# Optimization experiments

Measured on AMD Instinct MI355X. Metric: run time of the kernel, lower is better.

## Reference

```python
import jax, jax.numpy as jnp
import numpy as np
from jax import lax

B, N, C_IN, C_OUT = 4, 8192, 64, 128
STRIDE, RADIUS, K, L = 4, 0.1, 32, 2
EPS = 1e-5
M = N // STRIDE


def _bn(x, g, b):
    # training-mode batch norm, channel-first layout (B, C, ...)
    axes = (0,) + tuple(range(2, x.ndim))
    mean = jnp.mean(x, axis=axes, keepdims=True)
    var = jnp.mean((x - mean) ** 2, axis=axes, keepdims=True)
    sh = (1, -1) + (1,) * (x.ndim - 2)
    return (x - mean) * lax.rsqrt(var + EPS) * g.reshape(sh) + b.reshape(sh)


def _fps(points, m):
    # farthest point sampling starting at index 0 (matches fps_cuda semantics)
    b, n, _ = points.shape
    bi = jnp.arange(b)

    def body(carry, _):
        dis, last = carry
        lp = points[bi, last]  # (b,3)
        d = jnp.sum((points - lp[:, None, :]) ** 2, -1)
        dis = jnp.minimum(dis, d)
        return (dis, jnp.argmax(dis, -1).astype(jnp.int32)), last

    init = (jnp.full((b, n), 1e10, points.dtype), jnp.zeros((b,), jnp.int32))
    _, idx = lax.scan(body, init, None, length=m)
    return idx.T  # (b, m)


def _ball_query(radius, k, centroids, points, features):
    # first k points within radius of each centroid; pad with first hit
    b, n, _ = points.shape
    d2 = jnp.sum((centroids[:, :, None, :] - points[:, None, :, :]) ** 2, -1)  # (b,m,n)
    key = jnp.where(d2 < radius * radius, jnp.arange(n, dtype=jnp.int32), n)
    neg, _ = lax.top_k(-key, k)  # k smallest keys = first k in-ball indices
    sel = -neg  # (b,m,k)
    sel = jnp.where(sel == n, sel[..., :1], sel)
    sel = jnp.clip(sel, 0, n - 1)
    bi = jnp.arange(b)[:, None, None]
    gp = jnp.transpose(points[bi, sel], (0, 3, 2, 1))  # (b,3,k,m)
    gf = None
    if features is not None:
        gf = jnp.transpose(features[bi, sel], (0, 3, 2, 1))  # (b,c,k,m)
    return gp, gf


def _forward(pos, x, p):
    b, n, _ = pos.shape
    m = n // STRIDE
    bi = jnp.arange(b)[:, None]
    fps_idx = _fps(pos, m)
    centroids = pos[bi, fps_idx]  # (b,m,3)
    # x_mlp: 1x1 conv + BN + ReLU
    f = jax.nn.relu(_bn(jnp.einsum('bnc,oc->bon', x, p['W_x']), p['g_x'], p['b_x']))
    feats = jnp.transpose(f, (0, 2, 1))  # (b,n,C_OUT)
    gp, gf = _ball_query(RADIUS, K, centroids, pos, feats)
    cT = jnp.transpose(centroids, (0, 2, 1))[:, :, None, :]  # (b,3,1,m)
    gp = (gp - cT) / RADIUS
    gp = jax.nn.relu(_bn(jnp.einsum('bckm,oc->bokm', gp, p['W_ps']), p['g_ps'], p['b_ps']))
    xf = jnp.transpose(jnp.max(gf + gp, axis=2), (0, 2, 1))  # (b,m,C_OUT)
    # gen_pe on downsampled points
    R2 = RADIUS * 2
    gpe, _ = _ball_query(R2, K, centroids, centroids, None)
    gpe = (gpe - cT) / R2
    pe = jax.nn.relu(_bn(jnp.einsum('bckm,oc->bokm', gpe, p['W_pe']), p['g_pe'], p['b_pe']))
    # InvResMLP blocks
    for i in range(L):
        xc = jnp.transpose(xf, (0, 2, 1))  # (b,C,m)
        xc = jax.nn.relu(_bn(jnp.einsum('bcm,oc->bom', xc, p['W1'][i]), p['g1'][i], p['b1'][i]))
        feats_i = jnp.transpose(xc, (0, 2, 1))  # (b,m,C)
        _, gfi = _ball_query(R2, K, centroids, centroids, feats_i)
        g = jnp.max(gfi + pe, axis=2)  # (b,C,m)
        g = jax.nn.relu(_bn(jnp.einsum('bcm,oc->bom', g, p['W2a'][i]), p['g2a'][i], p['b2a'][i]))
        g = _bn(jnp.einsum('bcm,oc->bom', g, p['W2b'][i]), p['g2b'][i], p['b2b'][i])
        xf = jax.nn.relu(feats_i + jnp.transpose(g, (0, 2, 1)))
    return centroids, xf


def setup_inputs() -> dict:
    key = jax.random.key(0)
    ks = jax.random.split(key, 12)
    d = {
        'pos': jax.random.uniform(ks[0], (B, N, 3), jnp.float32),
        'x': jax.random.normal(ks[1], (B, N, C_IN), jnp.float32),
        'W_x': jax.random.normal(ks[2], (C_OUT, C_IN), jnp.float32) * 0.05,
        'g_x': jnp.ones((C_OUT,), jnp.float32), 'b_x': jnp.zeros((C_OUT,), jnp.float32),
        'W_ps': jax.random.normal(ks[3], (C_OUT, 3), jnp.float32) * 0.1,
        'g_ps': jnp.ones((C_OUT,), jnp.float32), 'b_ps': jnp.zeros((C_OUT,), jnp.float32),
        'W_pe': jax.random.normal(ks[4], (C_OUT, 3), jnp.float32) * 0.1,
        'g_pe': jnp.ones((C_OUT,), jnp.float32), 'b_pe': jnp.zeros((C_OUT,), jnp.float32),
        'W1': jax.random.normal(ks[5], (L, C_OUT, C_OUT), jnp.float32) * 0.05,
        'g1': jnp.ones((L, C_OUT), jnp.float32), 'b1': jnp.zeros((L, C_OUT), jnp.float32),
        'W2a': jax.random.normal(ks[6], (L, C_OUT, C_OUT), jnp.float32) * 0.05,
        'g2a': jnp.ones((L, C_OUT), jnp.float32), 'b2a': jnp.zeros((L, C_OUT), jnp.float32),
        'W2b': jax.random.normal(ks[7], (L, C_OUT, C_OUT), jnp.float32) * 0.05,
        'g2b': jnp.ones((L, C_OUT), jnp.float32), 'b2b': jnp.zeros((L, C_OUT), jnp.float32),
    }
    return d


def reference(pos, x, W_x, g_x, b_x, W_ps, g_ps, b_ps, W_pe, g_pe, b_pe,
              W1, g1, b1, W2a, g2a, b2a, W2b, g2b, b2b):
    p = dict(W_x=W_x, g_x=g_x, b_x=b_x, W_ps=W_ps, g_ps=g_ps, b_ps=b_ps,
             W_pe=W_pe, g_pe=g_pe, b_pe=b_pe, W1=W1, g1=g1, b1=b1,
             W2a=W2a, g2a=g2a, b2a=b2a, W2b=W2b, g2b=g2b, b2b=b2b)
    return _forward(pos, x, p)
```

## Files before the change

### kernel.cpp

```cpp
#include <hip/hip_runtime.h>


#define BB 4
#define NN 8192
#define MM 2048
#define HM 1024
#define KK 32
#define CI 64
#define CO 128
#define SG 16

typedef float vf2 __attribute__((ext_vector_type(2)));

#define ST_X 0
#define MO_PS 256
#define MO_PE 272
#define ST1 288
#define ST2A (288 + 2 * SG * 256)
#define ST2B (ST2A + 2 * SG * 256)
#define ST_TOTAL (ST2B + 512)

__device__ __forceinline__ float sq3(float dx, float dy, float dz) {
#pragma clang fp contract(off)
  return dx * dx + dy * dy + dz * dz;
}

__device__ __forceinline__ void fin_stats_d(const double* st, float gam,
                                            float bet, double cnt, int ch,
                                            float* sc, float* sh) {
  double mean = st[ch] / cnt;
  double var = st[128 + ch] / cnt - mean * mean;
  if (var < 0) var = 0;
  double s = (double)gam / sqrt(var + 1e-5);
  *sc = (float)s;
  *sh = (float)((double)bet - mean * s);
}

__device__ __forceinline__ void fin_grp_d(const double* st, float gam,
                                          float bet, double cnt, int ch,
                                          float* sc, float* sh) {
  double sum = 0, ssq = 0;
#pragma unroll
  for (int g = 0; g < SG; g++) {
    sum += st[g * 256 + ch];
    ssq += st[g * 256 + 128 + ch];
  }
  double mean = sum / cnt;
  double var = ssq / cnt - mean * mean;
  if (var < 0) var = 0;
  double s = (double)gam / sqrt(var + 1e-5);
  *sc = (float)s;
  *sh = (float)((double)bet - mean * s);
}

__device__ __forceinline__ void fin_mom_d(const double* mo, const float* Wrow,
                                          float gam, float bet, double cnt,
                                          float* sc, float* sh) {
  double w0 = Wrow[0], w1 = Wrow[1], w2 = Wrow[2];
  double mx = mo[0] / cnt, my = mo[1] / cnt, mz = mo[2] / cnt;
  double sxx = mo[3] / cnt, sxy = mo[4] / cnt, sxz = mo[5] / cnt;
  double syy = mo[6] / cnt, syz = mo[7] / cnt, szz = mo[8] / cnt;
  double mean = w0 * mx + w1 * my + w2 * mz;
  double ey2 = w0 * w0 * sxx + w1 * w1 * syy + w2 * w2 * szz +
               2.0 * (w0 * w1 * sxy + w0 * w2 * sxz + w1 * w2 * syz);
  double var = ey2 - mean * mean;
  if (var < 0) var = 0;
  double s = (double)gam / sqrt(var + 1e-5);
  *sc = (float)s;
  *sh = (float)((double)bet - mean * s);
}

template <int CTRL>
__device__ __forceinline__ int dpp_i(int v) {
  return __builtin_amdgcn_update_dpp(v, v, CTRL, 0xF, 0xF, false);
}
template <int CTRL>
__device__ __forceinline__ float dpp_f(float v) {
  return __int_as_float(dpp_i<CTRL>(__float_as_int(v)));
}

#define FT 512
#define NP 8
#define NW 8

__device__ __forceinline__ void bq_wave(int pair, const float* __restrict__ pts,
                                        int npts, float rsq, float inv_r,
                                        int* __restrict__ sel,
                                        const float* __restrict__ cent,
                                        int lane, int* __restrict__ s_selw,
                                        float* __restrict__ s_momw) {
  int b = pair >> 11;
  const float* P = pts + (size_t)b * npts * 3;
  const float* C = cent + (size_t)pair * 3;
  float cx = C[0], cy = C[1], cz = C[2];
  int cnt = 0;
  unsigned long long ltm = (1ull << lane) - 1ull;
  int nit = npts >> 8;
  for (int ch = 0; ch < nit; ch++) {
    int i0 = (ch << 8) + lane;
    bool h0, h1, h2, h3;
    {
      float a0 = P[i0 * 3 + 0], a1 = P[i0 * 3 + 1], a2 = P[i0 * 3 + 2];
      float b0 = P[(i0 + 64) * 3 + 0], b1 = P[(i0 + 64) * 3 + 1],
            b2 = P[(i0 + 64) * 3 + 2];
      float c0 = P[(i0 + 128) * 3 + 0], c1 = P[(i0 + 128) * 3 + 1],
            c2 = P[(i0 + 128) * 3 + 2];
      float e0 = P[(i0 + 192) * 3 + 0], e1 = P[(i0 + 192) * 3 + 1],
            e2 = P[(i0 + 192) * 3 + 2];
      h0 = sq3(a0 - cx, a1 - cy, a2 - cz) < rsq;
      h1 = sq3(b0 - cx, b1 - cy, b2 - cz) < rsq;
      h2 = sq3(c0 - cx, c1 - cy, c2 - cz) < rsq;
      h3 = sq3(e0 - cx, e1 - cy, e2 - cz) < rsq;
    }
    unsigned long long m0 = __ballot(h0);
    unsigned long long m1 = __ballot(h1);
    unsigned long long m2 = __ballot(h2);
    unsigned long long m3 = __ballot(h3);
    if (m0) {
      int k = cnt + __popcll(m0 & ltm);
      if (h0 && k < KK) s_selw[k] = i0;
      cnt += __popcll(m0);
    }
    if (m1) {
      int k = cnt + __popcll(m1 & ltm);
      if (h1 && k < KK) s_selw[k] = i0 + 64;
      cnt += __popcll(m1);
    }
    if (m2) {
      int k = cnt + __popcll(m2 & ltm);
      if (h2 && k < KK) s_selw[k] = i0 + 128;
      cnt += __popcll(m2);
    }
    if (m3) {
      int k = cnt + __popcll(m3 & ltm);
      if (h3 && k < KK) s_selw[k] = i0 + 192;
      cnt += __popcll(m3);
    }
    if (cnt >= KK) break;
  }
  int total = cnt < KK ? cnt : KK;
  int myidx = 0;
  if (lane < KK) {
    int v = (lane < total) ? s_selw[lane] : s_selw[0];
    sel[(size_t)pair * KK + lane] = v;
    myidx = v;
  }
  float gx = 0.f, gy = 0.f, gz = 0.f;
  if (lane < KK) {
    gx = (P[myidx * 3 + 0] - cx) * inv_r;
    gy = (P[myidx * 3 + 1] - cy) * inv_r;
    gz = (P[myidx * 3 + 2] - cz) * inv_r;
  }
  float v9[9] = {gx, gy, gz, gx * gx, gx * gy, gx * gz, gy * gy, gy * gz,
                 gz * gz};
#pragma unroll
  for (int j = 0; j < 9; j++) {
#pragma unroll
    for (int off = 32; off > 0; off >>= 1) v9[j] += __shfl_xor(v9[j], off);
  }
  if (lane == 0) {
#pragma unroll
    for (int j = 0; j < 9; j++) s_momw[j] = v9[j];
  }
}

__global__ __launch_bounds__(FT) void k_fps_conv(
    const float* __restrict__ pos, const float* __restrict__ x,
    const float* __restrict__ W_x, float* __restrict__ cent,
    float* __restrict__ fpre, double* __restrict__ stats,
    float* __restrict__ gds) {
  __shared__ alignas(16) unsigned long long s_key[2][NW];
  __shared__ alignas(16) float s_pts[NN * 3];
  __shared__ alignas(16) float s_cent[MM * 3];
  int t = threadIdx.x;
  if (blockIdx.x >= BB) {
    int cb = blockIdx.x - BB;
    int o = t & 127, q = t >> 7;
    float4 w[CI / 4];
    const float4* Wv = (const float4*)(W_x + (size_t)o * CI);
#pragma unroll
    for (int i = 0; i < CI / 4; i++) w[i] = Wv[i];
    int row0 = cb * 128;
    float ssum = 0.f, ssq = 0.f;
    for (int r = 0; r < 128; r += 4) {
      int row = __builtin_amdgcn_readfirstlane(row0 + r + q);
      const float* xr = x + (size_t)row * CI;
      float acc = 0.f;
#pragma unroll
      for (int i = 0; i < CI / 4; i++) {
        float4 a = *(const float4*)(xr + 4 * i);
        acc += a.x * w[i].x + a.y * w[i].y + a.z * w[i].z + a.w * w[i].w;
      }
      fpre[(size_t)row * CO + o] = acc;
      ssum += acc;
      ssq += acc * acc;
    }
    atomicAdd(&stats[ST_X + o], (double)ssum);
    atomicAdd(&stats[ST_X + 128 + o], (double)ssq);
    return;
  }
  int b = blockIdx.x;
  const float* P = pos + (size_t)b * NN * 3;
  float* C = cent + (size_t)b * MM * 3;
  int lane = t & 63, w = t >> 6;
  int ws = __builtin_amdgcn_readfirstlane(w);
  for (int i = t; i < (NN * 3) / 4; i += FT) {
    ((float4*)s_pts)[i] = ((const float4*)P)[i];
  }
  vf2 px[NP], py[NP], pz[NP], ds[NP];
#pragma unroll
  for (int s = 0; s < NP; s++) {
    int ia = (2 * s) * FT + t;
    int ib = ia + FT;
    px[s] = (vf2){P[ia * 3 + 0], P[ib * 3 + 0]};
    py[s] = (vf2){P[ia * 3 + 1], P[ib * 3 + 1]};
    pz[s] = (vf2){P[ia * 3 + 2], P[ib * 3 + 2]};
    ds[s] = (vf2){1e10f, 1e10f};
  }
  float lx = P[0], ly = P[1], lz = P[2];
  if (t == 0) {
    s_cent[0] = lx;
    s_cent[1] = ly;
    s_cent[2] = lz;
  }
  __syncthreads();
  for (int m = 1; m < HM; m++) {
    vf2 l2x = (vf2){lx, lx}, l2y = (vf2){ly, ly}, l2z = (vf2){lz, lz};
    vf2 bmax = (vf2){-1.0f, -1.0f};
    {
#pragma clang fp contract(off)
#pragma unroll
      for (int s = 0; s < NP; s++) {
        vf2 dx = px[s] - l2x;
        vf2 dy = py[s] - l2y;
        vf2 dz = pz[s] - l2z;
        vf2 d2 = dx * dx + dy * dy + dz * dz;
        vf2 nd = __builtin_elementwise_min(ds[s], d2);
        ds[s] = nd;
        bmax = __builtin_elementwise_max(bmax, nd);
      }
    }
    float bv = fmaxf(bmax.x, bmax.y);
    bv = fmaxf(bv, dpp_f<0x111>(bv));
    bv = fmaxf(bv, dpp_f<0x112>(bv));
    bv = fmaxf(bv, dpp_f<0x114>(bv));
    bv = fmaxf(bv, dpp_f<0x118>(bv));
    bv = fmaxf(bv, dpp_f<0x142>(bv));
    bv = fmaxf(bv, dpp_f<0x143>(bv));
    float wmax =
        __int_as_float(__builtin_amdgcn_readlane(__float_as_int(bv), 63));
    unsigned idxw = 0xffffffffu;
#pragma unroll
    for (int s = NP - 1; s >= 0; s--) {
      unsigned long long mby = __ballot(ds[s].y == wmax);
      unsigned basey = (unsigned)((2 * s) * FT + FT + (ws << 6));
      if (mby) idxw = basey + (unsigned)(__ffsll((long long)mby) - 1);
      unsigned long long mbx = __ballot(ds[s].x == wmax);
      unsigned basex = (unsigned)((2 * s) * FT + (ws << 6));
      if (mbx) idxw = basex + (unsigned)(__ffsll((long long)mbx) - 1);
    }
    int pb = m & 1;
    if (lane == 0) {
      s_key[pb][ws] = ((unsigned long long)__float_as_uint(wmax) << 32) |
                      (unsigned long long)(~idxw);
    }
    __syncthreads();
    const ulonglong2* kp = (const ulonglong2*)(&s_key[pb][0]);
    ulonglong2 q0 = kp[0];
    ulonglong2 q1 = kp[1];
    ulonglong2 q2 = kp[2];
    ulonglong2 q3 = kp[3];
    unsigned long long a0 = q0.x > q0.y ? q0.x : q0.y;
    unsigned long long a1 = q1.x > q1.y ? q1.x : q1.y;
    unsigned long long a2 = q2.x > q2.y ? q2.x : q2.y;
    unsigned long long a3 = q3.x > q3.y ? q3.x : q3.y;
    a0 = a0 > a1 ? a0 : a1;
    a2 = a2 > a3 ? a2 : a3;
    unsigned long long kw = a0 > a2 ? a0 : a2;
    unsigned gidx = ~(unsigned)(kw & 0xffffffffull);
    lx = s_pts[gidx * 3 + 0];
    ly = s_pts[gidx * 3 + 1];
    lz = s_pts[gidx * 3 + 2];
    if (t == 0) {
      s_cent[m * 3 + 0] = lx;
      s_cent[m * 3 + 1] = ly;
      s_cent[m * 3 + 2] = lz;
    }
  }
  __syncthreads();
  for (int i = t; i < (HM * 3) / 4; i += FT) {
    ((float4*)C)[i] = ((const float4*)s_cent)[i];
  }
  float2* gd = (float2*)gds + (size_t)b * NP * FT;
#pragma unroll
  for (int s = 0; s < NP; s++) {
    float2 v;
    v.x = ds[s].x;
    v.y = ds[s].y;
    gd[s * FT + t] = v;
  }
}

__global__ __launch_bounds__(FT) void k_fps_bq(const float* __restrict__ pos,
                                               float* __restrict__ cent,
                                               const float* __restrict__ gds,
                                               int* __restrict__ sel1,
                                               double* __restrict__ stats) {
  __shared__ alignas(16) unsigned long long s_key[2][NW];
  __shared__ alignas(16) float s_pts[NN * 3];
  __shared__ alignas(16) float s_cent[MM * 3];
  __shared__ int s_sel[NW][KK];
  __shared__ float s_mom[NW][9];
  int t = threadIdx.x;
  int lane = t & 63, w = t >> 6;
  if (blockIdx.x >= BB) {
    int pi = (blockIdx.x - BB) * 8 + w;
    int bb = pi >> 10, mi = pi & (HM - 1);
    int pair = bb * MM + mi;
    bq_wave(pair, pos, NN, 0.01f, 10.0f, sel1, cent, lane, s_sel[w],
            s_mom[w]);
    __syncthreads();
    if (t < 9) {
      double a = (double)s_mom[0][t];
#pragma unroll
      for (int j = 1; j < NW; j++) a += s_mom[j][t];
      atomicAdd(&stats[MO_PS + t], a);
    }
    return;
  }
  int b = blockIdx.x;
  const float* P = pos + (size_t)b * NN * 3;
  float* C = cent + (size_t)b * MM * 3;
  int ws = __builtin_amdgcn_readfirstlane(w);
  for (int i = t; i < (NN * 3) / 4; i += FT) {
    ((float4*)s_pts)[i] = ((const float4*)P)[i];
  }
  vf2 px[NP], py[NP], pz[NP], ds[NP];
  const float2* gd = (const float2*)gds + (size_t)b * NP * FT;
#pragma unroll
  for (int s = 0; s < NP; s++) {
    int ia = (2 * s) * FT + t;
    int ib = ia + FT;
    px[s] = (vf2){P[ia * 3 + 0], P[ib * 3 + 0]};
    py[s] = (vf2){P[ia * 3 + 1], P[ib * 3 + 1]};
    pz[s] = (vf2){P[ia * 3 + 2], P[ib * 3 + 2]};
    float2 v = gd[s * FT + t];
    ds[s] = (vf2){v.x, v.y};
  }
  float lx = C[(HM - 1) * 3 + 0];
  float ly = C[(HM - 1) * 3 + 1];
  float lz = C[(HM - 1) * 3 + 2];
  __syncthreads();
  for (int m = HM; m < MM; m++) {
    vf2 l2x = (vf2){lx, lx}, l2y = (vf2){ly, ly}, l2z = (vf2){lz, lz};
    vf2 bmax = (vf2){-1.0f, -1.0f};
    {
#pragma clang fp contract(off)
#pragma unroll
      for (int s = 0; s < NP; s++) {
        vf2 dx = px[s] - l2x;
        vf2 dy = py[s] - l2y;
        vf2 dz = pz[s] - l2z;
        vf2 d2 = dx * dx + dy * dy + dz * dz;
        vf2 nd = __builtin_elementwise_min(ds[s], d2);
        ds[s] = nd;
        bmax = __builtin_elementwise_max(bmax, nd);
      }
    }
    float bv = fmaxf(bmax.x, bmax.y);
    bv = fmaxf(bv, dpp_f<0x111>(bv));
    bv = fmaxf(bv, dpp_f<0x112>(bv));
    bv = fmaxf(bv, dpp_f<0x114>(bv));
    bv = fmaxf(bv, dpp_f<0x118>(bv));
    bv = fmaxf(bv, dpp_f<0x142>(bv));
    bv = fmaxf(bv, dpp_f<0x143>(bv));
    float wmax =
        __int_as_float(__builtin_amdgcn_readlane(__float_as_int(bv), 63));
    unsigned idxw = 0xffffffffu;
#pragma unroll
    for (int s = NP - 1; s >= 0; s--) {
      unsigned long long mby = __ballot(ds[s].y == wmax);
      unsigned basey = (unsigned)((2 * s) * FT + FT + (ws << 6));
      if (mby) idxw = basey + (unsigned)(__ffsll((long long)mby) - 1);
      unsigned long long mbx = __ballot(ds[s].x == wmax);
      unsigned basex = (unsigned)((2 * s) * FT + (ws << 6));
      if (mbx) idxw = basex + (unsigned)(__ffsll((long long)mbx) - 1);
    }
    int pb = m & 1;
    if (lane == 0) {
      s_key[pb][ws] = ((unsigned long long)__float_as_uint(wmax) << 32) |
                      (unsigned long long)(~idxw);
    }
    __syncthreads();
    const ulonglong2* kp = (const ulonglong2*)(&s_key[pb][0]);
    ulonglong2 q0 = kp[0];
    ulonglong2 q1 = kp[1];
    ulonglong2 q2 = kp[2];
    ulonglong2 q3 = kp[3];
    unsigned long long a0 = q0.x > q0.y ? q0.x : q0.y;
    unsigned long long a1 = q1.x > q1.y ? q1.x : q1.y;
    unsigned long long a2 = q2.x > q2.y ? q2.x : q2.y;
    unsigned long long a3 = q3.x > q3.y ? q3.x : q3.y;
    a0 = a0 > a1 ? a0 : a1;
    a2 = a2 > a3 ? a2 : a3;
    unsigned long long kw = a0 > a2 ? a0 : a2;
    unsigned gidx = ~(unsigned)(kw & 0xffffffffull);
    lx = s_pts[gidx * 3 + 0];
    ly = s_pts[gidx * 3 + 1];
    lz = s_pts[gidx * 3 + 2];
    if (t == 0) {
      s_cent[m * 3 + 0] = lx;
      s_cent[m * 3 + 1] = ly;
      s_cent[m * 3 + 2] = lz;
    }
  }
  __syncthreads();
  for (int i = t + (HM * 3) / 4; i < (MM * 3) / 4; i += FT) {
    ((float4*)C)[i] = ((const float4*)s_cent)[i];
  }
}

__global__ __launch_bounds__(256) void k_bq_rest(const float* __restrict__ pos,
                                                 const float* __restrict__ cent,
                                                 int* __restrict__ sel1,
                                                 int* __restrict__ sel2,
                                                 double* __restrict__ stats) {
  __shared__ int s_sel[4][KK];
  __shared__ float s_mom[4][9];
  int t = threadIdx.x, lane = t & 63, w = t >> 6;
  const float* pts;
  int npts, pair, mo;
  float rsq, inv_r;
  int* sel;
  if (blockIdx.x < (BB * HM) / 4) {
    int pi = blockIdx.x * 4 + w;
    int bb = pi >> 10, mi = pi & (HM - 1);
    pair = bb * MM + HM + mi;
    pts = pos;
    npts = NN;
    rsq = 0.01f;
    inv_r = 10.0f;
    sel = sel1;
    mo = MO_PS;
  } else {
    pair = (blockIdx.x - (BB * HM) / 4) * 4 + w;
    pts = cent;
    npts = MM;
    rsq = 0.04f;
    inv_r = 5.0f;
    sel = sel2;
    mo = MO_PE;
  }
  bq_wave(pair, pts, npts, rsq, inv_r, sel, cent, lane, s_sel[w], s_mom[w]);
  __syncthreads();
  if (t < 9) {
    double a = (double)s_mom[0][t] + s_mom[1][t] + s_mom[2][t] + s_mom[3][t];
    atomicAdd(&stats[mo + t], a);
  }
}

__global__ __launch_bounds__(128) void k_xf_conv1(
    const float* __restrict__ pos, const float* __restrict__ cent,
    const int* __restrict__ sel1, const float* __restrict__ fpre,
    const float* __restrict__ Wps, const float* __restrict__ g_ps,
    const float* __restrict__ b_ps, const float* __restrict__ g_x,
    const float* __restrict__ b_x, const double* __restrict__ stats,
    const float* __restrict__ W1, float* __restrict__ y1a,
    double* __restrict__ st1out) {
  int pair = blockIdx.x;
  int b = pair >> 11;
  int o = threadIdx.x;
  float sx, hx, sp, hp;
  fin_stats_d(stats + ST_X, g_x[o], b_x[o], (double)(BB * NN), o, &sx, &hx);
  fin_mom_d(stats + MO_PS, Wps + o * 3, g_ps[o], b_ps[o],
            (double)(BB * MM * KK), &sp, &hp);
  float w0 = Wps[o * 3 + 0], w1 = Wps[o * 3 + 1], w2 = Wps[o * 3 + 2];
  const float* C = cent + (size_t)pair * 3;
  float cx = C[0], cy = C[1], cz = C[2];
  const float* P = pos + (size_t)b * NN * 3;
  const float* F = fpre + (size_t)b * NN * CO;
  __shared__ int s_idx[KK];
  __shared__ float s_xf[128];
  if (o < KK) s_idx[o] = sel1[(size_t)pair * KK + o];
  __syncthreads();
  float acc = -1e30f;
#pragma unroll 4
  for (int k = 0; k < KK; k++) {
    int idx = __builtin_amdgcn_readfirstlane(s_idx[k]);
    float gx = (P[idx * 3 + 0] - cx) * 10.0f;
    float gy = (P[idx * 3 + 1] - cy) * 10.0f;
    float gz = (P[idx * 3 + 2] - cz) * 10.0f;
    float y = fmaxf((w0 * gx + w1 * gy + w2 * gz) * sp + hp, 0.f);
    float f = fmaxf(F[(size_t)idx * CO + o] * sx + hx, 0.f);
    float v = y + f;
    acc = v > acc ? v : acc;
  }
  s_xf[o] = acc;
  __syncthreads();
  const float4* Wv = (const float4*)(W1 + (size_t)o * CO);
  const float4* gv = (const float4*)s_xf;
  float dot = 0.f;
#pragma unroll
  for (int i = 0; i < CO / 4; i++) {
    float4 a = gv[i];
    float4 ww = Wv[i];
    dot += a.x * ww.x + a.y * ww.y + a.z * ww.z + a.w * ww.w;
  }
  y1a[(size_t)pair * CO + o] = dot;
  int grp = pair & (SG - 1);
  atomicAdd(&st1out[grp * 256 + o], (double)dot);
  atomicAdd(&st1out[grp * 256 + 128 + o], (double)(dot * dot));
}

__global__ __launch_bounds__(256) void k_conv_bnin(
    const float* __restrict__ in, const float* __restrict__ W,
    const double* __restrict__ st_grp, const float* __restrict__ gam,
    const float* __restrict__ bet, float* __restrict__ out,
    double* __restrict__ stats, int rows_per_block) {
  __shared__ float s_sc[128], s_sh[128];
  int t = threadIdx.x;
  if (t < 128) {
    fin_grp_d(st_grp, gam[t], bet[t], (double)(BB * MM), t, &s_sc[t],
              &s_sh[t]);
  }
  __syncthreads();
  int o = t & 127, half = t >> 7;
  float4 w[CO / 4];
  const float4* Wv = (const float4*)(W + (size_t)o * CO);
#pragma unroll
  for (int i = 0; i < CO / 4; i++) w[i] = Wv[i];
  int row0 = blockIdx.x * rows_per_block;
  float ssum = 0.f, ssq = 0.f;
  for (int r = 0; r < rows_per_block; r += 2) {
    int row = __builtin_amdgcn_readfirstlane(row0 + r + half);
    const float* xr = in + (size_t)row * CO;
    float acc = 0.f;
#pragma unroll
    for (int i = 0; i < CO / 4; i++) {
      float4 a = *(const float4*)(xr + 4 * i);
      a.x = fmaxf(a.x * s_sc[4 * i + 0] + s_sh[4 * i + 0], 0.f);
      a.y = fmaxf(a.y * s_sc[4 * i + 1] + s_sh[4 * i + 1], 0.f);
      a.z = fmaxf(a.z * s_sc[4 * i + 2] + s_sh[4 * i + 2], 0.f);
      a.w = fmaxf(a.w * s_sc[4 * i + 3] + s_sh[4 * i + 3], 0.f);
      acc += a.x * w[i].x + a.y * w[i].y + a.z * w[i].z + a.w * w[i].w;
    }
    out[(size_t)row * CO + o] = acc;
    ssum += acc;
    ssq += acc * acc;
  }
  atomicAdd(&stats[o], (double)ssum);
  atomicAdd(&stats[128 + o], (double)ssq);
}

__global__ __launch_bounds__(256) void k_conv_resid(
    const float* __restrict__ y1prev, const float* __restrict__ y2bprev,
    const double* __restrict__ st1p, const float* __restrict__ g1p,
    const float* __restrict__ b1p, const double* __restrict__ st2bp,
    const float* __restrict__ g2bp, const float* __restrict__ b2bp,
    const float* __restrict__ W, float* __restrict__ y1out,
    double* __restrict__ stats, int rows_per_block) {
  __shared__ float s_s1[128], s_h1[128], s_s2[128], s_h2[128];
  int t = threadIdx.x;
  if (t < 128) {
    fin_grp_d(st1p, g1p[t], b1p[t], (double)(BB * MM), t, &s_s1[t], &s_h1[t]);
    fin_stats_d(st2bp, g2bp[t], b2bp[t], (double)(BB * MM), t, &s_s2[t],
                &s_h2[t]);
  }
  __syncthreads();
  int o = t & 127, half = t >> 7;
  float4 w[CO / 4];
  const float4* Wv = (const float4*)(W + (size_t)o * CO);
#pragma unroll
  for (int i = 0; i < CO / 4; i++) w[i] = Wv[i];
  int row0 = blockIdx.x * rows_per_block;
  float ssum = 0.f, ssq = 0.f;
  for (int r = 0; r < rows_per_block; r += 2) {
    int row = __builtin_amdgcn_readfirstlane(row0 + r + half);
    const float* ar = y1prev + (size_t)row * CO;
    const float* br = y2bprev + (size_t)row * CO;
    float acc = 0.f;
#pragma unroll
    for (int i = 0; i < CO / 4; i++) {
      float4 a = *(const float4*)(ar + 4 * i);
      float4 bb = *(const float4*)(br + 4 * i);
      float x0 = fmaxf(fmaxf(a.x * s_s1[4 * i + 0] + s_h1[4 * i + 0], 0.f) +
                           (bb.x * s_s2[4 * i + 0] + s_h2[4 * i + 0]), 0.f);
      float x1 = fmaxf(fmaxf(a.y * s_s1[4 * i + 1] + s_h1[4 * i + 1], 0.f) +
                           (bb.y * s_s2[4 * i + 1] + s_h2[4 * i + 1]), 0.f);
      float x2 = fmaxf(fmaxf(a.z * s_s1[4 * i + 2] + s_h1[4 * i + 2], 0.f) +
                           (bb.z * s_s2[4 * i + 2] + s_h2[4 * i + 2]), 0.f);
      float x3 = fmaxf(fmaxf(a.w * s_s1[4 * i + 3] + s_h1[4 * i + 3], 0.f) +
                           (bb.w * s_s2[4 * i + 3] + s_h2[4 * i + 3]), 0.f);
      acc += x0 * w[i].x + x1 * w[i].y + x2 * w[i].z + x3 * w[i].w;
    }
    y1out[(size_t)row * CO + o] = acc;
    ssum += acc;
    ssq += acc * acc;
  }
  int grp = blockIdx.x & (SG - 1);
  atomicAdd(&stats[grp * 256 + o], (double)ssum);
  atomicAdd(&stats[grp * 256 + 128 + o], (double)ssq);
}

__global__ __launch_bounds__(128) void k_gconv(
    const float* __restrict__ cent, const int* __restrict__ sel2,
    const float* __restrict__ y1in, const double* __restrict__ st1,
    const float* __restrict__ g1v, const float* __restrict__ b1v,
    const double* __restrict__ mo_pe, const float* __restrict__ Wpe,
    const float* __restrict__ gpe, const float* __restrict__ bpe,
    const float* __restrict__ W2a, float* __restrict__ y2a,
    double* __restrict__ st2a) {
  int pair = blockIdx.x;
  int b = pair >> 11;
  int o = threadIdx.x;
  float s1, h1, se, he;
  fin_grp_d(st1, g1v[o], b1v[o], (double)(BB * MM), o, &s1, &h1);
  fin_mom_d(mo_pe, Wpe + o * 3, gpe[o], bpe[o], (double)(BB * MM * KK), &se,
            &he);
  float w0 = Wpe[o * 3 + 0], w1 = Wpe[o * 3 + 1], w2 = Wpe[o * 3 + 2];
  const float* C = cent + (size_t)pair * 3;
  float cx = C[0], cy = C[1], cz = C[2];
  const float* CB = cent + (size_t)b * MM * 3;
  const float* Y = y1in + (size_t)b * MM * CO;
  __shared__ int s_idx[KK];
  __shared__ float s_g[128];
  if (o < KK) s_idx[o] = sel2[(size_t)pair * KK + o];
  __syncthreads();
  float acc = -1e30f;
#pragma unroll 4
  for (int k = 0; k < KK; k++) {
    int idx = __builtin_amdgcn_readfirstlane(s_idx[k]);
    float gx = (CB[idx * 3 + 0] - cx) * 5.0f;
    float gy = (CB[idx * 3 + 1] - cy) * 5.0f;
    float gz = (CB[idx * 3 + 2] - cz) * 5.0f;
    float pe = fmaxf((w0 * gx + w1 * gy + w2 * gz) * se + he, 0.f);
    float f = fmaxf(Y[(size_t)idx * CO + o] * s1 + h1, 0.f);
    float v = pe + f;
    acc = v > acc ? v : acc;
  }
  s_g[o] = acc;
  __syncthreads();
  const float4* Wv = (const float4*)(W2a + (size_t)o * CO);
  const float4* gv = (const float4*)s_g;
  float dot = 0.f;
#pragma unroll
  for (int i = 0; i < CO / 4; i++) {
    float4 a = gv[i];
    float4 ww = Wv[i];
    dot += a.x * ww.x + a.y * ww.y + a.z * ww.z + a.w * ww.w;
  }
  y2a[(size_t)pair * CO + o] = dot;
  int grp = pair & (SG - 1);
  atomicAdd(&st2a[grp * 256 + o], (double)dot);
  atomicAdd(&st2a[grp * 256 + 128 + o], (double)(dot * dot));
}

__global__ __launch_bounds__(256) void k_resid_fin(
    const float* __restrict__ y1b, const double* __restrict__ st1,
    const float* __restrict__ g1v, const float* __restrict__ b1v,
    const float* __restrict__ y2b, const double* __restrict__ st2b,
    const float* __restrict__ g2bv, const float* __restrict__ b2bv,
    float* __restrict__ xf) {
  int i = blockIdx.x * 256 + threadIdx.x;
  int o = i & 127;
  float s1, h1, s2, h2;
  fin_grp_d(st1, g1v[o], b1v[o], (double)(BB * MM), o, &s1, &h1);
  fin_stats_d(st2b, g2bv[o], b2bv[o], (double)(BB * MM), o, &s2, &h2);
  float f = fmaxf(y1b[i] * s1 + h1, 0.f);
  float v = y2b[i] * s2 + h2;
  xf[i] = fmaxf(f + v, 0.f);
}

extern "C" void kernel_launch(void* const* d_in, const int* in_sizes, int n_in,
                              void* d_out, int out_size, void* d_ws,
                              size_t ws_size, hipStream_t stream) {
  const float* pos = (const float*)d_in[0];
  const float* x = (const float*)d_in[1];
  const float* W_x = (const float*)d_in[2];
  const float* g_x = (const float*)d_in[3];
  const float* b_x = (const float*)d_in[4];
  const float* W_ps = (const float*)d_in[5];
  const float* g_ps = (const float*)d_in[6];
  const float* b_ps = (const float*)d_in[7];
  const float* W_pe = (const float*)d_in[8];
  const float* g_pe = (const float*)d_in[9];
  const float* b_pe = (const float*)d_in[10];
  const float* W1 = (const float*)d_in[11];
  const float* g1 = (const float*)d_in[12];
  const float* b1 = (const float*)d_in[13];
  const float* W2a = (const float*)d_in[14];
  const float* g2a = (const float*)d_in[15];
  const float* b2a = (const float*)d_in[16];
  const float* W2b = (const float*)d_in[17];
  const float* g2b = (const float*)d_in[18];
  const float* b2b = (const float*)d_in[19];

  float* cent = (float*)d_out;
  float* xf = cent + (size_t)BB * MM * 3;

  char* p = (char*)d_ws;
  double* stats = (double*)p; p += (size_t)ST_TOTAL * sizeof(double);
  int* sel1 = (int*)p;        p += (size_t)BB * MM * KK * sizeof(int);
  int* sel2 = (int*)p;        p += (size_t)BB * MM * KK * sizeof(int);
  float* fpre = (float*)p;    p += (size_t)BB * NN * CO * sizeof(float);
  float* y1a = (float*)p;     p += (size_t)BB * MM * CO * sizeof(float);
  float* y1b = (float*)p;     p += (size_t)BB * MM * CO * sizeof(float);
  float* y2a = (float*)p;     p += (size_t)BB * MM * CO * sizeof(float);
  float* y2b = (float*)p;     p += (size_t)BB * MM * CO * sizeof(float);
  float* gds = (float*)p;     p += (size_t)BB * NP * FT * 2 * sizeof(float);

  hipMemsetAsync(stats, 0, (size_t)ST_TOTAL * sizeof(double), stream);
  k_fps_conv<<<BB + 256, FT, 0, stream>>>(pos, x, W_x, cent, fpre, stats, gds);
  k_fps_bq<<<BB + (BB * HM) / 8, FT, 0, stream>>>(pos, cent, gds, sel1, stats);
  k_bq_rest<<<(BB * HM) / 4 + (BB * MM) / 4, 256, 0, stream>>>(pos, cent, sel1,
                                                               sel2, stats);
  k_xf_conv1<<<BB * MM, 128, 0, stream>>>(pos, cent, sel1, fpre, W_ps, g_ps,
                                          b_ps, g_x, b_x, stats, W1, y1a,
                                          stats + ST1);
  k_gconv<<<BB * MM, 128, 0, stream>>>(cent, sel2, y1a, stats + ST1, g1, b1,
                                       stats + MO_PE, W_pe, g_pe, b_pe, W2a,
                                       y2a, stats + ST2A);
  k_conv_bnin<<<128, 256, 0, stream>>>(y2a, W2b, stats + ST2A, g2a, b2a, y2b,
                                       stats + ST2B, 64);
  k_conv_resid<<<128, 256, 0, stream>>>(
      y1a, y2b, stats + ST1, g1, b1, stats + ST2B, g2b, b2b, W1 + CO * CO, y1b,
      stats + ST1 + SG * 256, 64);
  k_gconv<<<BB * MM, 128, 0, stream>>>(cent, sel2, y1b, stats + ST1 + SG * 256,
                                       g1 + 128, b1 + 128, stats + MO_PE, W_pe,
                                       g_pe, b_pe, W2a + CO * CO, y2a,
                                       stats + ST2A + SG * 256);
  k_conv_bnin<<<128, 256, 0, stream>>>(y2a, W2b + CO * CO,
                                       stats + ST2A + SG * 256, g2a + 128,
                                       b2a + 128, y2b, stats + ST2B + 256, 64);
  k_resid_fin<<<(BB * MM * CO) / 256, 256, 0, stream>>>(
      y1b, stats + ST1 + SG * 256, g1 + 128, b1 + 128, y2b,
      stats + ST2B + 256, g2b + 128, b2b + 128, xf);
}
```

Before: 2.544 ms.

## Fuse tail stages into one cooperative persistent kernel with grid syncs

Replaces the eight tail kernels (remaining ball query, grouped convs, conv+BN layers, residual finalize) with one cooperative kernel of 256 blocks × 512 threads that steps through the stages separated by grid.sync. Each block now handles 32 pairs or rows, and per-block shared-memory reductions cut the number of double atomics on the stats buffers. The aim is to remove launch gaps and tail effects between many small kernels. In exchange, the grid is limited to 256 blocks, which lowers parallelism in the gather-heavy stages, and each stage boundary now costs a grid barrier.

```diff
diff --git a/kernel.cpp b/kernel.cpp
--- a/kernel.cpp
+++ b/kernel.cpp
@@ -1,4 +1,7 @@
 #include <hip/hip_runtime.h>
+#include <hip/hip_cooperative_groups.h>
+
+namespace cg = cooperative_groups;
 
 
 #define BB 4
@@ -9,6 +12,9 @@
 #define CI 64
 #define CO 128
 #define SG 16
+
+#define TB 256
+#define TT 512
 
 typedef float vf2 __attribute__((ext_vector_type(2)));
 
@@ -420,119 +426,102 @@
   }
 }
 
-__global__ __launch_bounds__(256) void k_bq_rest(const float* __restrict__ pos,
-                                                 const float* __restrict__ cent,
-                                                 int* __restrict__ sel1,
-                                                 int* __restrict__ sel2,
-                                                 double* __restrict__ stats) {
-  __shared__ int s_sel[4][KK];
-  __shared__ float s_mom[4][9];
-  int t = threadIdx.x, lane = t & 63, w = t >> 6;
-  const float* pts;
-  int npts, pair, mo;
-  float rsq, inv_r;
-  int* sel;
-  if (blockIdx.x < (BB * HM) / 4) {
-    int pi = blockIdx.x * 4 + w;
-    int bb = pi >> 10, mi = pi & (HM - 1);
-    pair = bb * MM + HM + mi;
-    pts = pos;
-    npts = NN;
-    rsq = 0.01f;
-    inv_r = 10.0f;
-    sel = sel1;
-    mo = MO_PS;
-  } else {
-    pair = (blockIdx.x - (BB * HM) / 4) * 4 + w;
-    pts = cent;
-    npts = MM;
-    rsq = 0.04f;
-    inv_r = 5.0f;
-    sel = sel2;
-    mo = MO_PE;
-  }
-  bq_wave(pair, pts, npts, rsq, inv_r, sel, cent, lane, s_sel[w], s_mom[w]);
+
+__device__ __forceinline__ void tail_gconv(
+    unsigned char* smem, int bid, int t, const float* __restrict__ cent,
+    const int* __restrict__ sel2, const float* __restrict__ yin,
+    const double* __restrict__ st1p, const float* __restrict__ g1v,
+    const float* __restrict__ b1v, const double* __restrict__ stats,
+    const float* __restrict__ Wpe, const float* __restrict__ gpe,
+    const float* __restrict__ bpe, const float* __restrict__ W2a_,
+    float* __restrict__ y2a_, double* __restrict__ st2a_) {
+  float* s_s1 = (float*)smem;
+  float* s_h1 = s_s1 + 128;
+  float* s_se = s_h1 + 128;
+  float* s_he = s_se + 128;
+  float* s_w0 = s_he + 128;
+  float* s_w1 = s_w0 + 128;
+  float* s_w2 = s_w1 + 128;
+  int* s_idx = (int*)(s_w2 + 128);
+  float* s_g = (float*)(s_idx + 4 * KK);
+  if (t < 128) {
+    float s1, h1, se, he;
+    fin_grp_d(st1p, g1v[t], b1v[t], (double)(BB * MM), t, &s1, &h1);
+    fin_mom_d(stats + MO_PE, Wpe + t * 3, gpe[t], bpe[t],
+              (double)(BB * MM * KK), &se, &he);
+    s_s1[t] = s1;
+    s_h1[t] = h1;
+    s_se[t] = se;
+    s_he[t] = he;
+    s_w0[t] = Wpe[t * 3 + 0];
+    s_w1[t] = Wpe[t * 3 + 1];
+    s_w2[t] = Wpe[t * 3 + 2];
+  }
   __syncthreads();
-  if (t < 9) {
-    double a = (double)s_mom[0][t] + s_mom[1][t] + s_mom[2][t] + s_mom[3][t];
-    atomicAdd(&stats[mo + t], a);
-  }
-}
-
-__global__ __launch_bounds__(128) void k_xf_conv1(
-    const float* __restrict__ pos, const float* __restrict__ cent,
-    const int* __restrict__ sel1, const float* __restrict__ fpre,
-    const float* __restrict__ Wps, const float* __restrict__ g_ps,
-    const float* __restrict__ b_ps, const float* __restrict__ g_x,
-    const float* __restrict__ b_x, const double* __restrict__ stats,
-    const float* __restrict__ W1, float* __restrict__ y1a,
-    double* __restrict__ st1out) {
-  int pair = blockIdx.x;
-  int b = pair >> 11;
-  int o = threadIdx.x;
-  float sx, hx, sp, hp;
-  fin_stats_d(stats + ST_X, g_x[o], b_x[o], (double)(BB * NN), o, &sx, &hx);
-  fin_mom_d(stats + MO_PS, Wps + o * 3, g_ps[o], b_ps[o],
-            (double)(BB * MM * KK), &sp, &hp);
-  float w0 = Wps[o * 3 + 0], w1 = Wps[o * 3 + 1], w2 = Wps[o * 3 + 2];
-  const float* C = cent + (size_t)pair * 3;
-  float cx = C[0], cy = C[1], cz = C[2];
-  const float* P = pos + (size_t)b * NN * 3;
-  const float* F = fpre + (size_t)b * NN * CO;
-  __shared__ int s_idx[KK];
-  __shared__ float s_xf[128];
-  if (o < KK) s_idx[o] = sel1[(size_t)pair * KK + o];
-  __syncthreads();
-  float acc = -1e30f;
+  int o = t & 127, sub = t >> 7;
+  float s1 = s_s1[o], h1 = s_h1[o], se = s_se[o], he = s_he[o];
+  float w0 = s_w0[o], w1 = s_w1[o], w2 = s_w2[o];
+  for (int p = 0; p < 8; p++) {
+    int pair = bid * 32 + p * 4 + sub;
+    int b = pair >> 11;
+    const float* C = cent + (size_t)pair * 3;
+    float cx = C[0], cy = C[1], cz = C[2];
+    const float* CB = cent + (size_t)b * MM * 3;
+    const float* Y = yin + (size_t)b * MM * CO;
+    if (o < KK) s_idx[sub * KK + o] = sel2[(size_t)pair * KK + o];
+    __syncthreads();
+    float acc = -1e30f;
 #pragma unroll 4
-  for (int k = 0; k < KK; k++) {
-    int idx = __builtin_amdgcn_readfirstlane(s_idx[k]);
-    float gx = (P[idx * 3 + 0] - cx) * 10.0f;
-    float gy = (P[idx * 3 + 1] - cy) * 10.0f;
-    float gz = (P[idx * 3 + 2] - cz) * 10.0f;
-    float y = fmaxf((w0 * gx + w1 * gy + w2 * gz) * sp + hp, 0.f);
-    float f = fmaxf(F[(size_t)idx * CO + o] * sx + hx, 0.f);
-    float v = y + f;
-    acc = v > acc ? v : acc;
-  }
-  s_xf[o] = acc;
-  __syncthreads();
-  const float4* Wv = (const float4*)(W1 + (size_t)o * CO);
-  const float4* gv = (const float4*)s_xf;
-  float dot = 0.f;
-#pragma unroll
-  for (int i = 0; i < CO / 4; i++) {
-    float4 a = gv[i];
-    float4 ww = Wv[i];
-    dot += a.x * ww.x + a.y * ww.y + a.z * ww.z + a.w * ww.w;
-  }
-  y1a[(size_t)pair * CO + o] = dot;
-  int grp = pair & (SG - 1);
-  atomicAdd(&st1out[grp * 256 + o], (double)dot);
-  atomicAdd(&st1out[grp * 256 + 128 + o], (double)(dot * dot));
-}
-
-__global__ __launch_bounds__(256) void k_conv_bnin(
-    const float* __restrict__ in, const float* __restrict__ W,
-    const double* __restrict__ st_grp, const float* __restrict__ gam,
-    const float* __restrict__ bet, float* __restrict__ out,
-    double* __restrict__ stats, int rows_per_block) {
-  __shared__ float s_sc[128], s_sh[128];
-  int t = threadIdx.x;
+    for (int k = 0; k < KK; k++) {
+      int idx = __builtin_amdgcn_readfirstlane(s_idx[sub * KK + k]);
+      float gx = (CB[idx * 3 + 0] - cx) * 5.0f;
+      float gy = (CB[idx * 3 + 1] - cy) * 5.0f;
+      float gz = (CB[idx * 3 + 2] - cz) * 5.0f;
+      float pe = fmaxf((w0 * gx + w1 * gy + w2 * gz) * se + he, 0.f);
+      float f = fmaxf(Y[(size_t)idx * CO + o] * s1 + h1, 0.f);
+      float v = pe + f;
+      acc = v > acc ? v : acc;
+    }
+    s_g[sub * 128 + o] = acc;
+    __syncthreads();
+    const float4* Wv = (const float4*)(W2a_ + (size_t)o * CO);
+    const float4* gv = (const float4*)(s_g + sub * 128);
+    float dot = 0.f;
+#pragma unroll
+    for (int i = 0; i < CO / 4; i++) {
+      float4 a = gv[i];
+      float4 ww = Wv[i];
+      dot += a.x * ww.x + a.y * ww.y + a.z * ww.z + a.w * ww.w;
+    }
+    y2a_[(size_t)pair * CO + o] = dot;
+    int grp = pair & (SG - 1);
+    atomicAdd(&st2a_[grp * 256 + o], (double)dot);
+    atomicAdd(&st2a_[grp * 256 + 128 + o], (double)(dot * dot));
+  }
+}
+
+__device__ __forceinline__ void tail_bnin(
+    unsigned char* smem, int bid, int t, const float* __restrict__ in,
+    const float* __restrict__ W, const double* __restrict__ st_grp,
+    const float* __restrict__ gam, const float* __restrict__ bet,
+    float* __restrict__ out, double* __restrict__ stat_out) {
+  float* s_sc = (float*)smem;
+  float* s_sh = s_sc + 128;
+  double* s_rs = (double*)(smem + 1024);
+  double* s_rq = s_rs + 512;
   if (t < 128) {
     fin_grp_d(st_grp, gam[t], bet[t], (double)(BB * MM), t, &s_sc[t],
               &s_sh[t]);
   }
   __syncthreads();
-  int o = t & 127, half = t >> 7;
+  int o = t & 127, oct = t >> 7;
   float4 w[CO / 4];
   const float4* Wv = (const float4*)(W + (size_t)o * CO);
 #pragma unroll
   for (int i = 0; i < CO / 4; i++) w[i] = Wv[i];
-  int row0 = blockIdx.x * rows_per_block;
   float ssum = 0.f, ssq = 0.f;
-  for (int r = 0; r < rows_per_block; r += 2) {
-    int row = __builtin_amdgcn_readfirstlane(row0 + r + half);
+  for (int r = 0; r < 32; r += 4) {
+    int row = __builtin_amdgcn_readfirstlane(bid * 32 + r + oct);
     const float* xr = in + (size_t)row * CO;
     float acc = 0.f;
 #pragma unroll
@@ -548,127 +537,222 @@
     ssum += acc;
     ssq += acc * acc;
   }
-  atomicAdd(&stats[o], (double)ssum);
-  atomicAdd(&stats[128 + o], (double)ssq);
-}
-
-__global__ __launch_bounds__(256) void k_conv_resid(
-    const float* __restrict__ y1prev, const float* __restrict__ y2bprev,
-    const double* __restrict__ st1p, const float* __restrict__ g1p,
-    const float* __restrict__ b1p, const double* __restrict__ st2bp,
-    const float* __restrict__ g2bp, const float* __restrict__ b2bp,
-    const float* __restrict__ W, float* __restrict__ y1out,
-    double* __restrict__ stats, int rows_per_block) {
-  __shared__ float s_s1[128], s_h1[128], s_s2[128], s_h2[128];
-  int t = threadIdx.x;
+  s_rs[oct * 128 + o] = (double)ssum;
+  s_rq[oct * 128 + o] = (double)ssq;
+  __syncthreads();
   if (t < 128) {
-    fin_grp_d(st1p, g1p[t], b1p[t], (double)(BB * MM), t, &s_s1[t], &s_h1[t]);
-    fin_stats_d(st2bp, g2bp[t], b2bp[t], (double)(BB * MM), t, &s_s2[t],
-                &s_h2[t]);
-  }
-  __syncthreads();
-  int o = t & 127, half = t >> 7;
-  float4 w[CO / 4];
-  const float4* Wv = (const float4*)(W + (size_t)o * CO);
-#pragma unroll
-  for (int i = 0; i < CO / 4; i++) w[i] = Wv[i];
-  int row0 = blockIdx.x * rows_per_block;
-  float ssum = 0.f, ssq = 0.f;
-  for (int r = 0; r < rows_per_block; r += 2) {
-    int row = __builtin_amdgcn_readfirstlane(row0 + r + half);
-    const float* ar = y1prev + (size_t)row * CO;
-    const float* br = y2bprev + (size_t)row * CO;
-    float acc = 0.f;
-#pragma unroll
-    for (int i = 0; i < CO / 4; i++) {
-      float4 a = *(const float4*)(ar + 4 * i);
-      float4 bb = *(const float4*)(br + 4 * i);
-      float x0 = fmaxf(fmaxf(a.x * s_s1[4 * i + 0] + s_h1[4 * i + 0], 0.f) +
-                           (bb.x * s_s2[4 * i + 0] + s_h2[4 * i + 0]), 0.f);
-      float x1 = fmaxf(fmaxf(a.y * s_s1[4 * i + 1] + s_h1[4 * i + 1], 0.f) +
-                           (bb.y * s_s2[4 * i + 1] + s_h2[4 * i + 1]), 0.f);
-      float x2 = fmaxf(fmaxf(a.z * s_s1[4 * i + 2] + s_h1[4 * i + 2], 0.f) +
-                           (bb.z * s_s2[4 * i + 2] + s_h2[4 * i + 2]), 0.f);
-      float x3 = fmaxf(fmaxf(a.w * s_s1[4 * i + 3] + s_h1[4 * i + 3], 0.f) +
-                           (bb.w * s_s2[4 * i + 3] + s_h2[4 * i + 3]), 0.f);
-      acc += x0 * w[i].x + x1 * w[i].y + x2 * w[i].z + x3 * w[i].w;
-    }
-    y1out[(size_t)row * CO + o] = acc;
-    ssum += acc;
-    ssq += acc * acc;
-  }
-  int grp = blockIdx.x & (SG - 1);
-  atomicAdd(&stats[grp * 256 + o], (double)ssum);
-  atomicAdd(&stats[grp * 256 + 128 + o], (double)ssq);
-}
-
-__global__ __launch_bounds__(128) void k_gconv(
-    const float* __restrict__ cent, const int* __restrict__ sel2,
-    const float* __restrict__ y1in, const double* __restrict__ st1,
-    const float* __restrict__ g1v, const float* __restrict__ b1v,
-    const double* __restrict__ mo_pe, const float* __restrict__ Wpe,
-    const float* __restrict__ gpe, const float* __restrict__ bpe,
-    const float* __restrict__ W2a, float* __restrict__ y2a,
-    double* __restrict__ st2a) {
-  int pair = blockIdx.x;
-  int b = pair >> 11;
-  int o = threadIdx.x;
-  float s1, h1, se, he;
-  fin_grp_d(st1, g1v[o], b1v[o], (double)(BB * MM), o, &s1, &h1);
-  fin_mom_d(mo_pe, Wpe + o * 3, gpe[o], bpe[o], (double)(BB * MM * KK), &se,
-            &he);
-  float w0 = Wpe[o * 3 + 0], w1 = Wpe[o * 3 + 1], w2 = Wpe[o * 3 + 2];
-  const float* C = cent + (size_t)pair * 3;
-  float cx = C[0], cy = C[1], cz = C[2];
-  const float* CB = cent + (size_t)b * MM * 3;
-  const float* Y = y1in + (size_t)b * MM * CO;
-  __shared__ int s_idx[KK];
-  __shared__ float s_g[128];
-  if (o < KK) s_idx[o] = sel2[(size_t)pair * KK + o];
-  __syncthreads();
-  float acc = -1e30f;
+    double a = s_rs[t] + s_rs[128 + t] + s_rs[256 + t] + s_rs[384 + t];
+    atomicAdd(&stat_out[t], a);
+  } else if (t < 256) {
+    int c = t - 128;
+    double a = s_rq[c] + s_rq[128 + c] + s_rq[256 + c] + s_rq[384 + c];
+    atomicAdd(&stat_out[128 + c], a);
+  }
+}
+
+__global__ __launch_bounds__(TT) void k_tail(
+    const float* __restrict__ pos, const float* __restrict__ cent,
+    int* __restrict__ sel1, int* __restrict__ sel2,
+    const float* __restrict__ fpre, const float* __restrict__ Wps,
+    const float* __restrict__ g_ps, const float* __restrict__ b_ps,
+    const float* __restrict__ g_x, const float* __restrict__ b_x,
+    const float* __restrict__ Wpe, const float* __restrict__ g_pe,
+    const float* __restrict__ b_pe, const float* __restrict__ W1,
+    const float* __restrict__ g1, const float* __restrict__ b1,
+    const float* __restrict__ W2a, const float* __restrict__ g2a,
+    const float* __restrict__ b2a, const float* __restrict__ W2b,
+    const float* __restrict__ g2b, const float* __restrict__ b2b,
+    double* __restrict__ stats, float* __restrict__ y1a,
+    float* __restrict__ y1b, float* __restrict__ y2a,
+    float* __restrict__ y2b, float* __restrict__ xf) {
+  cg::grid_group grid = cg::this_grid();
+  __shared__ alignas(16) unsigned char smem[10752];
+  int t = threadIdx.x, bid = blockIdx.x;
+  int lane = t & 63, w = t >> 6;
+  {
+    int* s_sel = (int*)smem;
+    float* s_mom = (float*)(smem + NW * KK * 4);
+    double dps = 0.0, dpe = 0.0;
+    for (int round = 0; round < 6; round++) {
+      int tid = round * (TB * NW) + bid * NW + w;
+      if (round < 2) {
+        int bb = tid >> 10, mi = tid & (HM - 1);
+        bq_wave(bb * MM + HM + mi, pos, NN, 0.01f, 10.0f, sel1, cent, lane,
+                s_sel + w * KK, s_mom + w * 9);
+      } else {
+        int pair = tid - 2 * (TB * NW);
+        bq_wave(pair, cent, MM, 0.04f, 5.0f, sel2, cent, lane, s_sel + w * KK,
+                s_mom + w * 9);
+      }
+      __syncthreads();
+      if (t < 9) {
+        double a = 0.0;
+#pragma unroll
+        for (int j = 0; j < NW; j++) a += (double)s_mom[j * 9 + t];
+        if (round < 2)
+          dps += a;
+        else
+          dpe += a;
+      }
+      __syncthreads();
+    }
+    if (t < 9) {
+      atomicAdd(&stats[MO_PS + t], dps);
+      atomicAdd(&stats[MO_PE + t], dpe);
+    }
+  }
+  grid.sync();
+  {
+    float* s_sx = (float*)smem;
+    float* s_hx = s_sx + 128;
+    float* s_sp = s_hx + 128;
+    float* s_hp = s_sp + 128;
+    float* s_w0 = s_hp + 128;
+    float* s_w1 = s_w0 + 128;
+    float* s_w2 = s_w1 + 128;
+    int* s_idx = (int*)(s_w2 + 128);
+    float* s_xf = (float*)(s_idx + 4 * KK);
+    if (t < 128) {
+      float sx, hx, sp, hp;
+      fin_stats_d(stats + ST_X, g_x[t], b_x[t], (double)(BB * NN), t, &sx,
+                  &hx);
+      fin_mom_d(stats + MO_PS, Wps + t * 3, g_ps[t], b_ps[t],
+                (double)(BB * MM * KK), &sp, &hp);
+      s_sx[t] = sx;
+      s_hx[t] = hx;
+      s_sp[t] = sp;
+      s_hp[t] = hp;
+      s_w0[t] = Wps[t * 3 + 0];
+      s_w1[t] = Wps[t * 3 + 1];
+      s_w2[t] = Wps[t * 3 + 2];
+    }
+    __syncthreads();
+    int o = t & 127, sub = t >> 7;
+    float sx = s_sx[o], hx = s_hx[o], sp = s_sp[o], hp = s_hp[o];
+    float w0 = s_w0[o], w1 = s_w1[o], w2 = s_w2[o];
+    for (int p = 0; p < 8; p++) {
+      int pair = bid * 32 + p * 4 + sub;
+      int b = pair >> 11;
+      const float* C = cent + (size_t)pair * 3;
+      float cx = C[0], cy = C[1], cz = C[2];
+      const float* P = pos + (size_t)b * NN * 3;
+      const float* F = fpre + (size_t)b * NN * CO;
+      if (o < KK) s_idx[sub * KK + o] = sel1[(size_t)pair * KK + o];
+      __syncthreads();
+      float acc = -1e30f;
 #pragma unroll 4
-  for (int k = 0; k < KK; k++) {
-    int idx = __builtin_amdgcn_readfirstlane(s_idx[k]);
-    float gx = (CB[idx * 3 + 0] - cx) * 5.0f;
-    float gy = (CB[idx * 3 + 1] - cy) * 5.0f;
-    float gz = (CB[idx * 3 + 2] - cz) * 5.0f;
-    float pe = fmaxf((w0 * gx + w1 * gy + w2 * gz) * se + he, 0.f);
-    float f = fmaxf(Y[(size_t)idx * CO + o] * s1 + h1, 0.f);
-    float v = pe + f;
-    acc = v > acc ? v : acc;
-  }
-  s_g[o] = acc;
-  __syncthreads();
-  const float4* Wv = (const float4*)(W2a + (size_t)o * CO);
-  const float4* gv = (const float4*)s_g;
-  float dot = 0.f;
-#pragma unroll
-  for (int i = 0; i < CO / 4; i++) {
-    float4 a = gv[i];
-    float4 ww = Wv[i];
-    dot += a.x * ww.x + a.y * ww.y + a.z * ww.z + a.w * ww.w;
-  }
-  y2a[(size_t)pair * CO + o] = dot;
-  int grp = pair & (SG - 1);
-  atomicAdd(&st2a[grp * 256 + o], (double)dot);
-  atomicAdd(&st2a[grp * 256 + 128 + o], (double)(dot * dot));
-}
-
-__global__ __launch_bounds__(256) void k_resid_fin(
-    const float* __restrict__ y1b, const double* __restrict__ st1,
-    const float* __restrict__ g1v, const float* __restrict__ b1v,
-    const float* __restrict__ y2b, const double* __restrict__ st2b,
-    const float* __restrict__ g2bv, const float* __restrict__ b2bv,
-    float* __restrict__ xf) {
-  int i = blockIdx.x * 256 + threadIdx.x;
-  int o = i & 127;
-  float s1, h1, s2, h2;
-  fin_grp_d(st1, g1v[o], b1v[o], (double)(BB * MM), o, &s1, &h1);
-  fin_stats_d(st2b, g2bv[o], b2bv[o], (double)(BB * MM), o, &s2, &h2);
-  float f = fmaxf(y1b[i] * s1 + h1, 0.f);
-  float v = y2b[i] * s2 + h2;
-  xf[i] = fmaxf(f + v, 0.f);
+      for (int k = 0; k < KK; k++) {
+        int idx = __builtin_amdgcn_readfirstlane(s_idx[sub * KK + k]);
+        float gx = (P[idx * 3 + 0] - cx) * 10.0f;
+        float gy = (P[idx * 3 + 1] - cy) * 10.0f;
+        float gz = (P[idx * 3 + 2] - cz) * 10.0f;
+        float y = fmaxf((w0 * gx + w1 * gy + w2 * gz) * sp + hp, 0.f);
+        float f = fmaxf(F[(size_t)idx * CO + o] * sx + hx, 0.f);
+        float v = y + f;
+        acc = v > acc ? v : acc;
+      }
+      s_xf[sub * 128 + o] = acc;
+      __syncthreads();
+      const float4* Wv = (const float4*)(W1 + (size_t)o * CO);
+      const float4* gv = (const float4*)(s_xf + sub * 128);
+      float dot = 0.f;
+#pragma unroll
+      for (int i = 0; i < CO / 4; i++) {
+        float4 a = gv[i];
+        float4 ww = Wv[i];
+        dot += a.x * ww.x + a.y * ww.y + a.z * ww.z + a.w * ww.w;
+      }
+      y1a[(size_t)pair * CO + o] = dot;
+      int grp = pair & (SG - 1);
+      atomicAdd(&stats[ST1 + grp * 256 + o], (double)dot);
+      atomicAdd(&stats[ST1 + grp * 256 + 128 + o], (double)(dot * dot));
+    }
+  }
+  grid.sync();
+  tail_gconv(smem, bid, t, cent, sel2, y1a, stats + ST1, g1, b1, stats, Wpe,
+             g_pe, b_pe, W2a, y2a, stats + ST2A);
+  grid.sync();
+  tail_bnin(smem, bid, t, y2a, W2b, stats + ST2A, g2a, b2a, y2b,
+            stats + ST2B);
+  grid.sync();
+  {
+    float* s_s1 = (float*)smem;
+    float* s_h1 = s_s1 + 128;
+    float* s_s2 = s_h1 + 128;
+    float* s_h2 = s_s2 + 128;
+    double* s_rs = (double*)(smem + 2048);
+    double* s_rq = s_rs + 512;
+    if (t < 128) {
+      fin_grp_d(stats + ST1, g1[t], b1[t], (double)(BB * MM), t, &s_s1[t],
+                &s_h1[t]);
+      fin_stats_d(stats + ST2B, g2b[t], b2b[t], (double)(BB * MM), t,
+                  &s_s2[t], &s_h2[t]);
+    }
+    __syncthreads();
+    int o = t & 127, oct = t >> 7;
+    float4 w[CO / 4];
+    const float4* Wv = (const float4*)(W1 + CO * CO + (size_t)o * CO);
+#pragma unroll
+    for (int i = 0; i < CO / 4; i++) w[i] = Wv[i];
+    float ssum = 0.f, ssq = 0.f;
+    for (int r = 0; r < 32; r += 4) {
+      int row = __builtin_amdgcn_readfirstlane(bid * 32 + r + oct);
+      const float* ar = y1a + (size_t)row * CO;
+      const float* br = y2b + (size_t)row * CO;
+      float acc = 0.f;
+#pragma unroll
+      for (int i = 0; i < CO / 4; i++) {
+        float4 a = *(const float4*)(ar + 4 * i);
+        float4 bb = *(const float4*)(br + 4 * i);
+        float x0 = fmaxf(fmaxf(a.x * s_s1[4 * i + 0] + s_h1[4 * i + 0], 0.f) +
+                             (bb.x * s_s2[4 * i + 0] + s_h2[4 * i + 0]), 0.f);
+        float x1 = fmaxf(fmaxf(a.y * s_s1[4 * i + 1] + s_h1[4 * i + 1], 0.f) +
+                             (bb.y * s_s2[4 * i + 1] + s_h2[4 * i + 1]), 0.f);
+        float x2 = fmaxf(fmaxf(a.z * s_s1[4 * i + 2] + s_h1[4 * i + 2], 0.f) +
+                             (bb.z * s_s2[4 * i + 2] + s_h2[4 * i + 2]), 0.f);
+        float x3 = fmaxf(fmaxf(a.w * s_s1[4 * i + 3] + s_h1[4 * i + 3], 0.f) +
+                             (bb.w * s_s2[4 * i + 3] + s_h2[4 * i + 3]), 0.f);
+        acc += x0 * w[i].x + x1 * w[i].y + x2 * w[i].z + x3 * w[i].w;
+      }
+      y1b[(size_t)row * CO + o] = acc;
+      ssum += acc;
+      ssq += acc * acc;
+    }
+    s_rs[oct * 128 + o] = (double)ssum;
+    s_rq[oct * 128 + o] = (double)ssq;
+    __syncthreads();
+    int grp = bid & (SG - 1);
+    if (t < 128) {
+      double a = s_rs[t] + s_rs[128 + t] + s_rs[256 + t] + s_rs[384 + t];
+      atomicAdd(&stats[ST1 + SG * 256 + grp * 256 + t], a);
+    } else if (t < 256) {
+      int c = t - 128;
+      double a = s_rq[c] + s_rq[128 + c] + s_rq[256 + c] + s_rq[384 + c];
+      atomicAdd(&stats[ST1 + SG * 256 + grp * 256 + 128 + c], a);
+    }
+  }
+  grid.sync();
+  tail_gconv(smem, bid, t, cent, sel2, y1b, stats + ST1 + SG * 256, g1 + 128,
+             b1 + 128, stats, Wpe, g_pe, b_pe, W2a + CO * CO, y2a,
+             stats + ST2A + SG * 256);
+  grid.sync();
+  tail_bnin(smem, bid, t, y2a, W2b + CO * CO, stats + ST2A + SG * 256,
+            g2a + 128, b2a + 128, y2b, stats + ST2B + 256);
+  grid.sync();
+  {
+    int o = t & 127;
+    float s1, h1, s2, h2;
+    fin_grp_d(stats + ST1 + SG * 256, g1[128 + o], b1[128 + o],
+              (double)(BB * MM), o, &s1, &h1);
+    fin_stats_d(stats + ST2B + 256, g2b[128 + o], b2b[128 + o],
+                (double)(BB * MM), o, &s2, &h2);
+    for (int r = 0; r < 8; r++) {
+      int i = bid * 4096 + r * 512 + t;
+      float f = fmaxf(y1b[i] * s1 + h1, 0.f);
+      float v = y2b[i] * s2 + h2;
+      xf[i] = fmaxf(f + v, 0.f);
+    }
+  }
 }
 
 extern "C" void kernel_launch(void* const* d_in, const int* in_sizes, int n_in,
@@ -712,27 +796,15 @@
   hipMemsetAsync(stats, 0, (size_t)ST_TOTAL * sizeof(double), stream);
   k_fps_conv<<<BB + 256, FT, 0, stream>>>(pos, x, W_x, cent, fpre, stats, gds);
   k_fps_bq<<<BB + (BB * HM) / 8, FT, 0, stream>>>(pos, cent, gds, sel1, stats);
-  k_bq_rest<<<(BB * HM) / 4 + (BB * MM) / 4, 256, 0, stream>>>(pos, cent, sel1,
-                                                               sel2, stats);
-  k_xf_conv1<<<BB * MM, 128, 0, stream>>>(pos, cent, sel1, fpre, W_ps, g_ps,
-                                          b_ps, g_x, b_x, stats, W1, y1a,
-                                          stats + ST1);
-  k_gconv<<<BB * MM, 128, 0, stream>>>(cent, sel2, y1a, stats + ST1, g1, b1,
-                                       stats + MO_PE, W_pe, g_pe, b_pe, W2a,
-                                       y2a, stats + ST2A);
-  k_conv_bnin<<<128, 256, 0, stream>>>(y2a, W2b, stats + ST2A, g2a, b2a, y2b,
-                                       stats + ST2B, 64);
-  k_conv_resid<<<128, 256, 0, stream>>>(
-      y1a, y2b, stats + ST1, g1, b1, stats + ST2B, g2b, b2b, W1 + CO * CO, y1b,
-      stats + ST1 + SG * 256, 64);
-  k_gconv<<<BB * MM, 128, 0, stream>>>(cent, sel2, y1b, stats + ST1 + SG * 256,
-                                       g1 + 128, b1 + 128, stats + MO_PE, W_pe,
-                                       g_pe, b_pe, W2a + CO * CO, y2a,
-                                       stats + ST2A + SG * 256);
-  k_conv_bnin<<<128, 256, 0, stream>>>(y2a, W2b + CO * CO,
-                                       stats + ST2A + SG * 256, g2a + 128,
-                                       b2a + 128, y2b, stats + ST2B + 256, 64);
-  k_resid_fin<<<(BB * MM * CO) / 256, 256, 0, stream>>>(
-      y1b, stats + ST1 + SG * 256, g1 + 128, b1 + 128, y2b,
-      stats + ST2B + 256, g2b + 128, b2b + 128, xf);
-}
+  {
+    void* args[] = {(void*)&pos, (void*)&cent, (void*)&sel1, (void*)&sel2,
+                    (void*)&fpre, (void*)&W_ps, (void*)&g_ps, (void*)&b_ps,
+                    (void*)&g_x, (void*)&b_x, (void*)&W_pe, (void*)&g_pe,
+                    (void*)&b_pe, (void*)&W1, (void*)&g1, (void*)&b1,
+                    (void*)&W2a, (void*)&g2a, (void*)&b2a, (void*)&W2b,
+                    (void*)&g2b, (void*)&b2b, (void*)&stats, (void*)&y1a,
+                    (void*)&y1b, (void*)&y2a, (void*)&y2b, (void*)&xf};
+    hipLaunchCooperativeKernel((void*)k_tail, dim3(TB), dim3(TT), args, 0,
+                               stream);
+  }
+}
```

Measured after the change: 2.852 ms. 1.12x slower.
